# Optimization experiments

Hardware: AMD Instinct MI355X
Metric: run time of the kernel (lower is better)

The kernel has to match this reference:

```python
import jax, jax.numpy as jnp
import numpy as np

N = 4096
IN_F = 256
OUT_F = 64
HEADS = 8
ALPHA = 0.2  # LeakyReLU negative slope


def setup_inputs() -> dict:
    key = jax.random.key(0)
    k1, k2, k3, k4 = jax.random.split(key, 4)
    X = jax.random.normal(k1, (N, IN_F), dtype=jnp.float32)
    adj = jax.random.randint(k2, (N, N), 0, 2, dtype=jnp.int32)
    # self-loops so every row has at least one neighbor (softmax well-defined)
    idx = jnp.arange(N)
    adj = adj.at[idx, idx].set(1)
    W = jax.random.normal(k3, (HEADS, IN_F, OUT_F), dtype=jnp.float32) * 0.05
    a = jax.random.normal(k4, (HEADS, 2 * OUT_F, 1), dtype=jnp.float32) * 0.05
    return {"X": X, "adj": adj, "W": W, "a": a}


def reference(X, adj, W, a):
    # H: [heads, N, F]
    H = jnp.einsum('ni,hio->hno', X, W)
    F_ = H.shape[-1]
    # cat([h_i, h_j]) @ a  ==  h_i @ a[:F] + h_j @ a[F:]
    a1 = a[:, :F_, 0]   # [heads, F]
    a2 = a[:, F_:, 0]   # [heads, F]
    f1 = jnp.einsum('hnf,hf->hn', H, a1)  # score contribution of row node i
    f2 = jnp.einsum('hnf,hf->hn', H, a2)  # score contribution of col node j
    e = jax.nn.leaky_relu(f1[:, :, None] + f2[:, None, :], negative_slope=ALPHA)  # [heads, N, N]
    e = jnp.where(adj[None, :, :] == 0, -jnp.inf, e)
    attention = jax.nn.softmax(e, axis=-1)
    # dropout omitted (eval mode)
    H_out = jnp.einsum('hnm,hmf->hnf', attention, H)  # [heads, N, F]
    return H_out.mean(axis=0)  # [N, F]
```

## Files before the change

### kernel.cpp

```cpp
#include <hip/hip_runtime.h>
#include <hip/hip_bf16.h>

#define N_NODES 4096
#define IN_F 256
#define OUT_F 64
#define HEADS 8
#define ALPHA 0.2f

typedef _Float16 f16x8 __attribute__((ext_vector_type(8)));
typedef float f32x4 __attribute__((ext_vector_type(4)));
union U4 { uint4 u; f16x8 h; unsigned w[4]; };

#define BFRAG_OFF 0
#define F1_OFF    (BFRAG_OFF + 8*128*4*64*8*2)
#define GP_OFF    (F1_OFF + 8*4096*4)
#define GN_OFF    (GP_OFF + 8*4096*2)
#define ADJ_OFF   (GN_OFF + 8*4096*2)

static __device__ __forceinline__ unsigned pkmul(unsigned a, unsigned b) {
  unsigned r; asm("v_pk_mul_f16 %0, %1, %2" : "=v"(r) : "v"(a), "v"(b)); return r;
}
static __device__ __forceinline__ unsigned pkmax(unsigned a, unsigned b) {
  unsigned r; asm("v_pk_max_f16 %0, %1, %2" : "=v"(r) : "v"(a), "v"(b)); return r;
}
static __device__ __forceinline__ unsigned pkadd(unsigned a, unsigned b) {
  unsigned r; asm("v_pk_add_f16 %0, %1, %2" : "=v"(r) : "v"(a), "v"(b)); return r;
}
static __device__ __forceinline__ unsigned short f2h_bits(float f) {
  return __builtin_bit_cast(unsigned short, (_Float16)f);
}
static __device__ __forceinline__ float h2f(unsigned short x) {
  return (float)__builtin_bit_cast(_Float16, x);
}

__global__ __launch_bounds__(256) void k_all(
    const float* __restrict__ X, const int* __restrict__ adj,
    const float* __restrict__ W, const float* __restrict__ a,
    unsigned long long* __restrict__ bits, _Float16* __restrict__ bfrag,
    float* __restrict__ f1, _Float16* __restrict__ Gp, _Float16* __restrict__ Gn,
    float* __restrict__ out) {
  __shared__ _Float16 wf[16384];
  int b = blockIdx.x, t = threadIdx.x;
  if (b < 2048) {
    int lane = t & 63;
    int waveid = b * 4 + (t >> 6);
    for (int it = 0; it < 32; ++it) {
      int widx = waveid + it * 8192;
      int v = adj[(size_t)widx * 64 + lane];
      unsigned long long m = __ballot(v != 0);
      if (lane == 0) bits[widx] = m;
    }
    return;
  }
  int b2 = b - 2048;
  int h = b2 >> 6, rb = b2 & 63;
  const float* Wh = W + (size_t)h * 16384;
  for (int q = t; q < 16384; q += 256) {
    float wv = Wh[q];
    int k = q >> 6, f = q & 63;
    int kt = k >> 5, lg = (k >> 3) & 3, e = k & 7;
    int ct = f >> 4, lr = f & 15;
    wf[(size_t)(((kt*4 + ct)*64) + lg*16 + lr) * 8 + e] = (_Float16)wv;
  }
  __syncthreads();
  int w = t >> 6, l = t & 63;
  int i0 = rb * 64 + w * 16;
  int r = l & 15, g = l >> 4;
  f32x4 z = {0.f, 0.f, 0.f, 0.f};
  f32x4 acc[4] = {z, z, z, z};
#pragma unroll
  for (int kt = 0; kt < 8; ++kt) {
    const float4* xr = (const float4*)(X + (size_t)(i0 + r) * 256 + (kt*4 + g) * 8);
    float4 x0 = xr[0], x1 = xr[1];
    U4 af;
    af.h[0] = (_Float16)x0.x; af.h[1] = (_Float16)x0.y;
    af.h[2] = (_Float16)x0.z; af.h[3] = (_Float16)x0.w;
    af.h[4] = (_Float16)x1.x; af.h[5] = (_Float16)x1.y;
    af.h[6] = (_Float16)x1.z; af.h[7] = (_Float16)x1.w;
#pragma unroll
    for (int ct = 0; ct < 4; ++ct) {
      U4 bv = *(const U4*)(wf + (size_t)(((kt*4 + ct)*64) + l) * 8);
      acc[ct] = __builtin_amdgcn_mfma_f32_16x16x32_f16(af.h, bv.h, acc[ct], 0, 0, 0);
    }
  }
  int jb = i0 + g*4;
#pragma unroll
  for (int ct = 0; ct < 4; ++ct) {
    size_t base = ((((size_t)h*128 + (jb>>5))*4 + ct)*64 + ((jb>>3)&3)*16 + r) * 8
                  + (jb & 7);
    union { short4 s; _Float16 hh[4]; } sv;
#pragma unroll
    for (int ri = 0; ri < 4; ++ri) sv.hh[ri] = (_Float16)acc[ct][ri];
    *(short4*)(bfrag + base) = sv.s;
  }
  float a1v[4], a2v[4];
#pragma unroll
  for (int ct = 0; ct < 4; ++ct) {
    a1v[ct] = a[h*128 + ct*16 + r];
    a2v[ct] = a[h*128 + 64 + ct*16 + r];
  }
#pragma unroll
  for (int ri = 0; ri < 4; ++ri) {
    float s1 = acc[0][ri]*a1v[0] + acc[1][ri]*a1v[1]
             + acc[2][ri]*a1v[2] + acc[3][ri]*a1v[3];
    float s2 = acc[0][ri]*a2v[0] + acc[1][ri]*a2v[1]
             + acc[2][ri]*a2v[2] + acc[3][ri]*a2v[3];
#pragma unroll
    for (int off = 1; off < 16; off <<= 1) {
      s1 += __shfl_xor(s1, off);
      s2 += __shfl_xor(s2, off);
    }
    if (r == 0) {
      int row = i0 + g*4 + ri;
      f1[h*4096 + row] = s1;
      Gp[h*4096 + row] = (_Float16)__expf(s2);
      Gn[h*4096 + row] = (_Float16)__expf(ALPHA * s2);
    }
  }
  if (h == 0) {
    float4* oz = (float4*)(out + (size_t)(rb * 64) * 64);
    float4 zz = make_float4(0.f, 0.f, 0.f, 0.f);
    for (int q = t; q < 1024; q += 256) oz[q] = zz;
  }
}

#define ATTN_BODY(PF, JT, DOPF) {                                              \
  U4 gp, gn;                                                                   \
  gp.u = Gs0[(JT)*4 + g].u;                                                    \
  gn.u = Gs1[(JT)*4 + g].u;                                                    \
  U4 b0, b1, b2, b3;                                                           \
  b0.u = PF[0]; b1.u = PF[1]; b2.u = PF[2]; b3.u = PF[3];                      \
  _Pragma("unroll")                                                            \
  for (int rg = 0; rg < 2; ++rg) {                                             \
    unsigned wm = Lb[rh32 + rg*16 + r][JT];                                    \
    U4 av;                                                                     \
    _Pragma("unroll")                                                          \
    for (int p = 0; p < 4; ++p) {                                              \
      unsigned pm = pkmax(pkmul(Epp[rg], gp.w[p]), pkmul(Enn[rg], gn.w[p]));   \
      av.w[p] = pm & MLUT[(wm >> (g8 + 2*p)) & 3u];                            \
    }                                                                          \
    acc[rg][0] = __builtin_amdgcn_mfma_f32_16x16x32_f16(av.h, b0.h, acc[rg][0], 0,0,0); \
    acc[rg][1] = __builtin_amdgcn_mfma_f32_16x16x32_f16(av.h, b1.h, acc[rg][1], 0,0,0); \
    acc[rg][2] = __builtin_amdgcn_mfma_f32_16x16x32_f16(av.h, b2.h, acc[rg][2], 0,0,0); \
    acc[rg][3] = __builtin_amdgcn_mfma_f32_16x16x32_f16(av.h, b3.h, acc[rg][3], 0,0,0); \
    unsigned sden = pkadd(pkadd(av.w[0], av.w[1]), pkadd(av.w[2], av.w[3]));   \
    den[rg] += h2f((unsigned short)(sden & 0xFFFFu))                           \
             + h2f((unsigned short)(sden >> 16));                              \
  }                                                                            \
  if (DOPF) {                                                                  \
    _Pragma("unroll")                                                          \
    for (int c = 0; c < 4; ++c) PF[c] = bfh[((JT) + 2)*256 + c*64];            \
  }                                                                            \
}

#define WRBUF(i) {                                                             \
  _Pragma("unroll")                                                            \
  for (int rg = 0; rg < 2; ++rg)                                               \
    _Pragma("unroll")                                                          \
    for (int ct = 0; ct < 4; ++ct) redp[(i)*576 + (rg*4+ct)*64 + l] = acc[rg][ct]; \
  f32x4 dv = {den[0], den[1], 0.f, 0.f};                                       \
  redp[(i)*576 + 512 + l] = dv;                                                \
}
#define ADBUF(i) {                                                             \
  _Pragma("unroll")                                                            \
  for (int rg = 0; rg < 2; ++rg)                                               \
    _Pragma("unroll")                                                          \
    for (int ct = 0; ct < 4; ++ct) acc[rg][ct] += redp[(i)*576 + (rg*4+ct)*64 + l]; \
  f32x4 dv = redp[(i)*576 + 512 + l];                                          \
  den[0] += dv[0]; den[1] += dv[1];                                            \
}

__global__ __launch_bounds__(512, 4) void k_attn(
    const float* __restrict__ f1, const unsigned int* __restrict__ adjbits,
    const _Float16* __restrict__ Gp, const _Float16* __restrict__ Gn,
    const _Float16* __restrict__ bfrag, float* __restrict__ out) {
  __shared__ __align__(16) char smem[49408];
  __shared__ unsigned MLUT[4];
  unsigned (*Lb)[129] = (unsigned(*)[129])smem;
  U4* Gs0 = (U4*)(smem + 33024);
  U4* Gs1 = (U4*)(smem + 41216);
  f32x4* redp = (f32x4*)smem;
  int b = blockIdx.x;
  int h = b & 7, rs = b >> 3;
  int i0 = rs * 64;
  int t = threadIdx.x, wid = t >> 6, l = t & 63;
  int rh = wid >> 2, jq = wid & 3;
  int rh32 = rh * 32;
  int r = l & 15, g = l >> 4, g8 = g * 8;
  if (t < 4) MLUT[t] = ((t & 1) ? 0xFFFFu : 0u) | ((t & 2) ? 0xFFFF0000u : 0u);
  const uint4* bfh = (const uint4*)bfrag + (size_t)h * 32768 + l;
  int jt0 = jq * 32;
  uint4 pA[4], pB[4];
#pragma unroll
  for (int c = 0; c < 4; ++c) pA[c] = bfh[jt0 * 256 + c*64];
#pragma unroll
  for (int c = 0; c < 4; ++c) pB[c] = bfh[(jt0 + 1) * 256 + c*64];
  for (int q = t; q < 8192; q += 512)
    Lb[q >> 7][q & 127] = adjbits[(size_t)(i0 + (q >> 7)) * 128 + (q & 127)];
  Gs0[t].u = ((const uint4*)(Gp + (size_t)h * 4096))[t];
  Gs1[t].u = ((const uint4*)(Gn + (size_t)h * 4096))[t];
  unsigned Epp[2], Enn[2];
#pragma unroll
  for (int rg = 0; rg < 2; ++rg) {
    float f1r = f1[h * N_NODES + i0 + rh32 + rg*16 + r];
    unsigned short ep = f2h_bits(__expf(f1r));
    unsigned short en = f2h_bits(__expf(ALPHA * f1r));
    Epp[rg] = ep | ((unsigned)ep << 16);
    Enn[rg] = en | ((unsigned)en << 16);
  }
  __syncthreads();
  f32x4 z = {0.f,0.f,0.f,0.f};
  f32x4 acc[2][4] = {{z,z,z,z},{z,z,z,z}};
  float den[2] = {0.f, 0.f};
  for (int q2 = 0; q2 < 16; ++q2) {
    ATTN_BODY(pA, jt0 + q2*2,     (q2 < 15));
    ATTN_BODY(pB, jt0 + q2*2 + 1, (q2 < 15));
  }
  __syncthreads();
  if (jq == 1 || jq == 3) WRBUF(rh*2 + (jq >> 1));
  __syncthreads();
  if (jq == 0) ADBUF(rh*2);
  if (jq == 2) ADBUF(rh*2 + 1);
  __syncthreads();
  if (jq == 2) WRBUF(rh);
  __syncthreads();
  if (jq == 0) {
    ADBUF(rh);
#pragma unroll
    for (int rg = 0; rg < 2; ++rg) {
      den[rg] += __shfl_xor(den[rg], 16);
      den[rg] += __shfl_xor(den[rg], 32);
    }
#pragma unroll
    for (int rg = 0; rg < 2; ++rg)
#pragma unroll
      for (int ri = 0; ri < 4; ++ri) {
        float dr = __shfl(den[rg], g*4 + ri);
        float sc = 0.125f / dr;
        float* op = out + (size_t)(i0 + rh32 + rg*16 + g*4 + ri) * 64;
        atomicAdd(op + r,      acc[rg][0][ri] * sc);
        atomicAdd(op + 16 + r, acc[rg][1][ri] * sc);
        atomicAdd(op + 32 + r, acc[rg][2][ri] * sc);
        atomicAdd(op + 48 + r, acc[rg][3][ri] * sc);
      }
  }
}

extern "C" void kernel_launch(void* const* d_in, const int* in_sizes, int n_in,
                              void* d_out, int out_size, void* d_ws, size_t ws_size,
                              hipStream_t stream) {
  const float* X = (const float*)d_in[0];
  const int* adj = (const int*)d_in[1];
  const float* W = (const float*)d_in[2];
  const float* a = (const float*)d_in[3];
  float* out = (float*)d_out;
  char* ws = (char*)d_ws;

  _Float16* bfrag = (_Float16*)(ws + BFRAG_OFF);
  float* f1 = (float*)(ws + F1_OFF);
  _Float16* Gp = (_Float16*)(ws + GP_OFF);
  _Float16* Gn = (_Float16*)(ws + GN_OFF);
  unsigned long long* bits64 = (unsigned long long*)(ws + ADJ_OFF);
  const unsigned int* bits32 = (const unsigned int*)(ws + ADJ_OFF);

  k_all<<<dim3(2560), dim3(256), 0, stream>>>(X, adj, W, a, bits64, bfrag,
                                              f1, Gp, Gn, out);
  k_attn<<<dim3(512), dim3(512), 0, stream>>>(f1, bits32, Gp, Gn, bfrag, out);
}
```

Before: 77.78 us.

## Prepack W fragments once, reorder adjacency packing, widen attention waves to 64 rows

Adds a small pre-kernel that converts W to fp16 MFMA fragment layout once and zeroes the output. The projection blocks then read the packed fragments directly instead of having every block re-convert all of W into shared memory. The adjacency bit-packing blocks move after the projection blocks, and each wave batches four nontemporal loads and ballots at a time. In the attention kernel each wave now covers all 64 rows with 4 waves per block (256 threads) instead of 32 rows with 8 waves, so each B fragment feeds twice as many MFMAs, at the cost of more accumulator registers and an extra kernel launch.

```diff
diff --git a/kernel.cpp b/kernel.cpp
--- a/kernel.cpp
+++ b/kernel.cpp
@@ -11,7 +11,8 @@
 typedef float f32x4 __attribute__((ext_vector_type(4)));
 union U4 { uint4 u; f16x8 h; unsigned w[4]; };
 
-#define BFRAG_OFF 0
+#define WFRAG_OFF 0
+#define BFRAG_OFF (WFRAG_OFF + 8*8*4*64*8*2)
 #define F1_OFF    (BFRAG_OFF + 8*128*4*64*8*2)
 #define GP_OFF    (F1_OFF + 8*4096*4)
 #define GN_OFF    (GP_OFF + 8*4096*2)
@@ -33,39 +34,60 @@
   return (float)__builtin_bit_cast(_Float16, x);
 }
 
-__global__ __launch_bounds__(256) void k_all(
+__global__ __launch_bounds__(256) void k_pre(const float* __restrict__ W,
+                                             _Float16* __restrict__ wfrag,
+                                             float* __restrict__ out) {
+  int b = blockIdx.x, t = threadIdx.x;
+  if (b < 8) {
+    int h = b;
+    for (int pos = t; pos < 2048; pos += 256) {
+      int kt = pos >> 8, ct = (pos >> 6) & 3, l = pos & 63;
+      int lr = l & 15, lg = l >> 4;
+#pragma unroll
+      for (int e = 0; e < 8; ++e)
+        wfrag[(size_t)(((h*8 + kt)*4 + ct)*64 + l) * 8 + e]
+          = (_Float16)W[(size_t)(h*256 + kt*32 + lg*8 + e) * 64 + ct*16 + lr];
+    }
+  } else {
+    float4* oz = ((float4*)out) + (size_t)(b - 8) * 8192;
+    float4 zz = make_float4(0.f, 0.f, 0.f, 0.f);
+    for (int q = t; q < 8192; q += 256) oz[q] = zz;
+  }
+}
+
+__global__ __launch_bounds__(256) void k_main(
     const float* __restrict__ X, const int* __restrict__ adj,
-    const float* __restrict__ W, const float* __restrict__ a,
+    const _Float16* __restrict__ wfrag, const float* __restrict__ a,
     unsigned long long* __restrict__ bits, _Float16* __restrict__ bfrag,
-    float* __restrict__ f1, _Float16* __restrict__ Gp, _Float16* __restrict__ Gn,
-    float* __restrict__ out) {
-  __shared__ _Float16 wf[16384];
+    float* __restrict__ f1, _Float16* __restrict__ Gp, _Float16* __restrict__ Gn) {
   int b = blockIdx.x, t = threadIdx.x;
-  if (b < 2048) {
+  if (b >= 512) {
+    int b2 = b - 512;
     int lane = t & 63;
-    int waveid = b * 4 + (t >> 6);
-    for (int it = 0; it < 32; ++it) {
-      int widx = waveid + it * 8192;
-      int v = adj[(size_t)widx * 64 + lane];
-      unsigned long long m = __ballot(v != 0);
-      if (lane == 0) bits[widx] = m;
+    int waveid = b2 * 4 + (t >> 6);
+#pragma unroll
+    for (int it2 = 0; it2 < 8; ++it2) {
+      int w0 = waveid + (it2*4 + 0) * 8192;
+      int w1 = waveid + (it2*4 + 1) * 8192;
+      int w2 = waveid + (it2*4 + 2) * 8192;
+      int w3 = waveid + (it2*4 + 3) * 8192;
+      int v0 = __builtin_nontemporal_load(adj + (size_t)w0 * 64 + lane);
+      int v1 = __builtin_nontemporal_load(adj + (size_t)w1 * 64 + lane);
+      int v2 = __builtin_nontemporal_load(adj + (size_t)w2 * 64 + lane);
+      int v3 = __builtin_nontemporal_load(adj + (size_t)w3 * 64 + lane);
+      unsigned long long m0 = __ballot(v0 != 0);
+      unsigned long long m1 = __ballot(v1 != 0);
+      unsigned long long m2 = __ballot(v2 != 0);
+      unsigned long long m3 = __ballot(v3 != 0);
+      if (lane == 0) { bits[w0] = m0; bits[w1] = m1; bits[w2] = m2; bits[w3] = m3; }
     }
     return;
   }
-  int b2 = b - 2048;
-  int h = b2 >> 6, rb = b2 & 63;
-  const float* Wh = W + (size_t)h * 16384;
-  for (int q = t; q < 16384; q += 256) {
-    float wv = Wh[q];
-    int k = q >> 6, f = q & 63;
-    int kt = k >> 5, lg = (k >> 3) & 3, e = k & 7;
-    int ct = f >> 4, lr = f & 15;
-    wf[(size_t)(((kt*4 + ct)*64) + lg*16 + lr) * 8 + e] = (_Float16)wv;
-  }
-  __syncthreads();
+  int h = b & 7, rb = b >> 3;
   int w = t >> 6, l = t & 63;
   int i0 = rb * 64 + w * 16;
   int r = l & 15, g = l >> 4;
+  const U4* wv = (const U4*)wfrag;
   f32x4 z = {0.f, 0.f, 0.f, 0.f};
   f32x4 acc[4] = {z, z, z, z};
 #pragma unroll
@@ -79,7 +101,7 @@
     af.h[6] = (_Float16)x1.z; af.h[7] = (_Float16)x1.w;
 #pragma unroll
     for (int ct = 0; ct < 4; ++ct) {
-      U4 bv = *(const U4*)(wf + (size_t)(((kt*4 + ct)*64) + l) * 8);
+      U4 bv = wv[((h*8 + kt)*4 + ct)*64 + l];
       acc[ct] = __builtin_amdgcn_mfma_f32_16x16x32_f16(af.h, bv.h, acc[ct], 0, 0, 0);
     }
   }
@@ -116,11 +138,6 @@
       Gp[h*4096 + row] = (_Float16)__expf(s2);
       Gn[h*4096 + row] = (_Float16)__expf(ALPHA * s2);
     }
-  }
-  if (h == 0) {
-    float4* oz = (float4*)(out + (size_t)(rb * 64) * 64);
-    float4 zz = make_float4(0.f, 0.f, 0.f, 0.f);
-    for (int q = t; q < 1024; q += 256) oz[q] = zz;
   }
 }
 
@@ -131,8 +148,8 @@
   U4 b0, b1, b2, b3;                                                           \
   b0.u = PF[0]; b1.u = PF[1]; b2.u = PF[2]; b3.u = PF[3];                      \
   _Pragma("unroll")                                                            \
-  for (int rg = 0; rg < 2; ++rg) {                                             \
-    unsigned wm = Lb[rh32 + rg*16 + r][JT];                                    \
+  for (int rg = 0; rg < 4; ++rg) {                                             \
+    unsigned wm = Lb[rg*16 + r][JT];                                           \
     U4 av;                                                                     \
     _Pragma("unroll")                                                          \
     for (int p = 0; p < 4; ++p) {                                              \
@@ -155,22 +172,22 @@
 
 #define WRBUF(i) {                                                             \
   _Pragma("unroll")                                                            \
-  for (int rg = 0; rg < 2; ++rg)                                               \
-    _Pragma("unroll")                                                          \
-    for (int ct = 0; ct < 4; ++ct) redp[(i)*576 + (rg*4+ct)*64 + l] = acc[rg][ct]; \
-  f32x4 dv = {den[0], den[1], 0.f, 0.f};                                       \
-  redp[(i)*576 + 512 + l] = dv;                                                \
+  for (int rg = 0; rg < 4; ++rg)                                               \
+    _Pragma("unroll")                                                          \
+    for (int ct = 0; ct < 4; ++ct) redp[(i)*1088 + (rg*4+ct)*64 + l] = acc[rg][ct]; \
+  f32x4 dv = {den[0], den[1], den[2], den[3]};                                 \
+  redp[(i)*1088 + 1024 + l] = dv;                                              \
 }
 #define ADBUF(i) {                                                             \
   _Pragma("unroll")                                                            \
-  for (int rg = 0; rg < 2; ++rg)                                               \
-    _Pragma("unroll")                                                          \
-    for (int ct = 0; ct < 4; ++ct) acc[rg][ct] += redp[(i)*576 + (rg*4+ct)*64 + l]; \
-  f32x4 dv = redp[(i)*576 + 512 + l];                                          \
-  den[0] += dv[0]; den[1] += dv[1];                                            \
-}
-
-__global__ __launch_bounds__(512, 4) void k_attn(
+  for (int rg = 0; rg < 4; ++rg)                                               \
+    _Pragma("unroll")                                                          \
+    for (int ct = 0; ct < 4; ++ct) acc[rg][ct] += redp[(i)*1088 + (rg*4+ct)*64 + l]; \
+  f32x4 dv = redp[(i)*1088 + 1024 + l];                                        \
+  den[0] += dv[0]; den[1] += dv[1]; den[2] += dv[2]; den[3] += dv[3];          \
+}
+
+__global__ __launch_bounds__(256, 3) void k_attn(
     const float* __restrict__ f1, const unsigned int* __restrict__ adjbits,
     const _Float16* __restrict__ Gp, const _Float16* __restrict__ Gn,
     const _Float16* __restrict__ bfrag, float* __restrict__ out) {
@@ -183,9 +200,7 @@
   int b = blockIdx.x;
   int h = b & 7, rs = b >> 3;
   int i0 = rs * 64;
-  int t = threadIdx.x, wid = t >> 6, l = t & 63;
-  int rh = wid >> 2, jq = wid & 3;
-  int rh32 = rh * 32;
+  int t = threadIdx.x, jq = t >> 6, l = t & 63;
   int r = l & 15, g = l >> 4, g8 = g * 8;
   if (t < 4) MLUT[t] = ((t & 1) ? 0xFFFFu : 0u) | ((t & 2) ? 0xFFFF0000u : 0u);
   const uint4* bfh = (const uint4*)bfrag + (size_t)h * 32768 + l;
@@ -195,14 +210,20 @@
   for (int c = 0; c < 4; ++c) pA[c] = bfh[jt0 * 256 + c*64];
 #pragma unroll
   for (int c = 0; c < 4; ++c) pB[c] = bfh[(jt0 + 1) * 256 + c*64];
-  for (int q = t; q < 8192; q += 512)
+  for (int q = t; q < 8192; q += 256)
     Lb[q >> 7][q & 127] = adjbits[(size_t)(i0 + (q >> 7)) * 128 + (q & 127)];
-  Gs0[t].u = ((const uint4*)(Gp + (size_t)h * 4096))[t];
-  Gs1[t].u = ((const uint4*)(Gn + (size_t)h * 4096))[t];
-  unsigned Epp[2], Enn[2];
-#pragma unroll
-  for (int rg = 0; rg < 2; ++rg) {
-    float f1r = f1[h * N_NODES + i0 + rh32 + rg*16 + r];
+  {
+    const uint4* gp4 = (const uint4*)(Gp + (size_t)h * 4096);
+    const uint4* gn4 = (const uint4*)(Gn + (size_t)h * 4096);
+    for (int q = t; q < 512; q += 256) {
+      Gs0[q].u = gp4[q];
+      Gs1[q].u = gn4[q];
+    }
+  }
+  unsigned Epp[4], Enn[4];
+#pragma unroll
+  for (int rg = 0; rg < 4; ++rg) {
+    float f1r = f1[h * N_NODES + i0 + rg*16 + r];
     unsigned short ep = f2h_bits(__expf(f1r));
     unsigned short en = f2h_bits(__expf(ALPHA * f1r));
     Epp[rg] = ep | ((unsigned)ep << 16);
@@ -210,34 +231,35 @@
   }
   __syncthreads();
   f32x4 z = {0.f,0.f,0.f,0.f};
-  f32x4 acc[2][4] = {{z,z,z,z},{z,z,z,z}};
-  float den[2] = {0.f, 0.f};
+  f32x4 acc[4][4] = {{z,z,z,z},{z,z,z,z},{z,z,z,z},{z,z,z,z}};
+  float den[4] = {0.f, 0.f, 0.f, 0.f};
   for (int q2 = 0; q2 < 16; ++q2) {
     ATTN_BODY(pA, jt0 + q2*2,     (q2 < 15));
     ATTN_BODY(pB, jt0 + q2*2 + 1, (q2 < 15));
   }
   __syncthreads();
-  if (jq == 1 || jq == 3) WRBUF(rh*2 + (jq >> 1));
-  __syncthreads();
-  if (jq == 0) ADBUF(rh*2);
-  if (jq == 2) ADBUF(rh*2 + 1);
-  __syncthreads();
-  if (jq == 2) WRBUF(rh);
+  if (jq == 1) WRBUF(0);
+  if (jq == 3) WRBUF(1);
+  __syncthreads();
+  if (jq == 0) ADBUF(0);
+  if (jq == 2) ADBUF(1);
+  __syncthreads();
+  if (jq == 2) WRBUF(0);
   __syncthreads();
   if (jq == 0) {
-    ADBUF(rh);
-#pragma unroll
-    for (int rg = 0; rg < 2; ++rg) {
+    ADBUF(0);
+#pragma unroll
+    for (int rg = 0; rg < 4; ++rg) {
       den[rg] += __shfl_xor(den[rg], 16);
       den[rg] += __shfl_xor(den[rg], 32);
     }
 #pragma unroll
-    for (int rg = 0; rg < 2; ++rg)
+    for (int rg = 0; rg < 4; ++rg)
 #pragma unroll
       for (int ri = 0; ri < 4; ++ri) {
         float dr = __shfl(den[rg], g*4 + ri);
         float sc = 0.125f / dr;
-        float* op = out + (size_t)(i0 + rh32 + rg*16 + g*4 + ri) * 64;
+        float* op = out + (size_t)(i0 + rg*16 + g*4 + ri) * 64;
         atomicAdd(op + r,      acc[rg][0][ri] * sc);
         atomicAdd(op + 16 + r, acc[rg][1][ri] * sc);
         atomicAdd(op + 32 + r, acc[rg][2][ri] * sc);
@@ -256,6 +278,7 @@
   float* out = (float*)d_out;
   char* ws = (char*)d_ws;
 
+  _Float16* wfrag = (_Float16*)(ws + WFRAG_OFF);
   _Float16* bfrag = (_Float16*)(ws + BFRAG_OFF);
   float* f1 = (float*)(ws + F1_OFF);
   _Float16* Gp = (_Float16*)(ws + GP_OFF);
@@ -263,7 +286,8 @@
   unsigned long long* bits64 = (unsigned long long*)(ws + ADJ_OFF);
   const unsigned int* bits32 = (const unsigned int*)(ws + ADJ_OFF);
 
-  k_all<<<dim3(2560), dim3(256), 0, stream>>>(X, adj, W, a, bits64, bfrag,
-                                              f1, Gp, Gn, out);
-  k_attn<<<dim3(512), dim3(512), 0, stream>>>(f1, bits32, Gp, Gn, bfrag, out);
-}
+  k_pre<<<dim3(16), dim3(256), 0, stream>>>(W, wfrag, out);
+  k_main<<<dim3(2560), dim3(256), 0, stream>>>(X, adj, wfrag, a, bits64, bfrag,
+                                               f1, Gp, Gn);
+  k_attn<<<dim3(512), dim3(256), 0, stream>>>(f1, bits32, Gp, Gn, bfrag, out);
+}
```

Result: faster. 74.69 us (-4.0%).
